# Optimization experiments

Measured on AMD Instinct MI355X. Metric: run time of the kernel, lower is better.

## Reference

```python
import jax, jax.numpy as jnp
import numpy as np

N = 8192
C = 128
K = 20          # neighbors per dilation branch
DILS = (1, 2)   # dilations
K_FULL = K * max(DILS)  # neighbors in the base knn graph
R = 4           # upsampling ratio
N_IDGCN = 2     # inception blocks
NEG_SLOPE_CONV = 0.2
NEG_SLOPE_MLP = 0.01  # torch LeakyReLU default in reconstructor


def knn_idx(pos, k):
    # brute-force knn on [N,3]; exclude self by taking k+1 and dropping col 0
    sq = jnp.sum(pos * pos, axis=-1)                       # [N]
    d = sq[:, None] + sq[None, :] - 2.0 * (pos @ pos.T)    # [N,N]
    _, idx = jax.lax.top_k(-d, k + 1)                      # nearest first
    return idx[:, 1:]                                      # [N,k]


def edge_conv(x, idx, W, b):
    # EdgeConv: max_j LeakyReLU(W @ [x_i, x_j - x_i] + b)
    xj = x[idx]                                            # [N,k,C] gather
    xi = jnp.broadcast_to(x[:, None, :], xj.shape)
    e = jnp.concatenate([xi, xj - xi], axis=-1)            # [N,k,2C]
    h = jax.nn.leaky_relu(e @ W + b, NEG_SLOPE_CONV)
    return jnp.max(h, axis=1)                              # [N,Cout]


def setup_inputs() -> dict:
    key = jax.random.key(0)
    ks = jax.random.split(key, 10)
    s_lift = 1.0 / np.sqrt(6.0)
    s_gcn = 1.0 / np.sqrt(2.0 * C)
    s_mlp = 1.0 / np.sqrt(C)
    n_gcn = N_IDGCN * len(DILS)
    return {
        "x": jax.random.normal(ks[0], (N, 3), dtype=jnp.float32),
        "W0": jax.random.normal(ks[1], (6, C), dtype=jnp.float32) * s_lift,
        "b0": jnp.zeros((C,), dtype=jnp.float32),
        "Wg": jax.random.normal(ks[2], (n_gcn, 2 * C, C), dtype=jnp.float32) * s_gcn,
        "bg": jnp.zeros((n_gcn, C), dtype=jnp.float32),
        "Wu": jax.random.normal(ks[3], (2 * C, R * C), dtype=jnp.float32) * s_gcn,
        "bu": jnp.zeros((R * C,), dtype=jnp.float32),
        "Wr1": jax.random.normal(ks[4], (C, C), dtype=jnp.float32) * s_mlp,
        "br1": jnp.zeros((C,), dtype=jnp.float32),
        "Wr2": jax.random.normal(ks[5], (C, 3), dtype=jnp.float32) * s_mlp,
        "br2": jnp.zeros((3,), dtype=jnp.float32),
    }


def reference(x, W0, b0, Wg, bg, Wu, bu, Wr1, br1, Wr2, br2):
    pos = x
    # knn graph on positions (k * max(dilations) neighbors)
    idx = knn_idx(pos, K_FULL)                             # [N, K_FULL]
    # lift 3 -> C with an EdgeConv on the first K neighbors
    h = edge_conv(pos, idx[:, :K], W0, b0)                 # [N, C]
    # Inception DenseGCN feature extractor: dilated EdgeConv branches + residual
    li = 0
    for _ in range(N_IDGCN):
        acc = jnp.zeros_like(h)
        for d in DILS:
            idx_d = idx[:, ::d][:, :K]                     # dilated neighbors
            acc = acc + edge_conv(h, idx_d, Wg[li], bg[li])
            li += 1
        h = h + acc / float(len(DILS))                     # residual
    # NodeShuffle upsampler: EdgeConv to r*C then shuffle nodes
    u = edge_conv(h, idx[:, :K], Wu, bu)                   # [N, r*C]
    u = u.reshape(N * R, C)                                # [N*r, C]
    # reconstructor MLP -> 3D coordinates
    q = jax.nn.leaky_relu(u @ Wr1 + br1, NEG_SLOPE_MLP)
    q = q @ Wr2 + br2                                      # [N*r, 3]
    return q
```

## Files before the change

### kernel.cpp

```cpp
#include <hip/hip_runtime.h>
#include <math.h>

#define N_PTS 8192
#define KFULL 40
#define KNB 20
#define QB 8
#define NBUCK 1024
#define HWORDS (NBUCK + NBUCK / 16)
#define CAP 384

typedef unsigned short u16;
typedef unsigned int u32;
typedef unsigned long long u64;
typedef __attribute__((ext_vector_type(8))) short bf16x8;
typedef __attribute__((ext_vector_type(4))) float f32x4;

__device__ __forceinline__ u16 f2b(float v) {
  u32 u = __float_as_uint(v);
  return (u16)((u + 0x7FFFu + ((u >> 16) & 1u)) >> 16);
}
__device__ __forceinline__ u32 pk2(float a, float b) {
  return (u32)f2b(a) | ((u32)f2b(b) << 16);
}
__device__ __forceinline__ u32 dmap(float d) {
  u32 b = __float_as_uint(d);
  return b ^ ((u32)(((int)b) >> 31) | 0x80000000u);
}
__device__ __forceinline__ void maxu4(const uint4 v, float m[8]) {
  m[0] = fmaxf(m[0], __uint_as_float(v.x << 16));
  m[1] = fmaxf(m[1], __uint_as_float(v.x & 0xFFFF0000u));
  m[2] = fmaxf(m[2], __uint_as_float(v.y << 16));
  m[3] = fmaxf(m[3], __uint_as_float(v.y & 0xFFFF0000u));
  m[4] = fmaxf(m[4], __uint_as_float(v.z << 16));
  m[5] = fmaxf(m[5], __uint_as_float(v.z & 0xFFFF0000u));
  m[6] = fmaxf(m[6], __uint_as_float(v.w << 16));
  m[7] = fmaxf(m[7], __uint_as_float(v.w & 0xFFFF0000u));
}
__device__ __forceinline__ void unp4(const uint4 v, float p[8]) {
  p[0] = __uint_as_float(v.x << 16);
  p[1] = __uint_as_float(v.x & 0xFFFF0000u);
  p[2] = __uint_as_float(v.y << 16);
  p[3] = __uint_as_float(v.y & 0xFFFF0000u);
  p[4] = __uint_as_float(v.z << 16);
  p[5] = __uint_as_float(v.z & 0xFFFF0000u);
  p[6] = __uint_as_float(v.w << 16);
  p[7] = __uint_as_float(v.w & 0xFFFF0000u);
}

typedef const __attribute__((address_space(1))) unsigned int* gas_p;
typedef __attribute__((address_space(3))) unsigned int* las_p;
__device__ __forceinline__ void gll16(const void* g, void* l) {
  __builtin_amdgcn_global_load_lds((gas_p)g, (las_p)l, 16, 0, 0);
}

__global__ __launch_bounds__(256) void pos4_kernel(const float* __restrict__ pos,
                                                   float4* __restrict__ pos4) {
  const int j = blockIdx.x * 256 + threadIdx.x;
  const float x = pos[j * 3 + 0], y = pos[j * 3 + 1], z = pos[j * 3 + 2];
  pos4[j] = make_float4(x, y, z, x * x + y * y + z * z);
}

__device__ __forceinline__ void scan_cut(const u32 (*hist)[HWORDS], int* s_cut,
                                         int t) {
  const int w = t >> 6, lane = t & 63;
  const u32* H = hist[w];
  const int base = lane * 17;
  u32 lsum = 0;
#pragma unroll
  for (int k = 0; k < 16; ++k) lsum += H[base + k];
  u32 inc = lsum;
#pragma unroll
  for (int off = 1; off < 64; off <<= 1) {
    const u32 u = __shfl_up(inc, off);
    if (lane >= off) inc += u;
  }
  const u32 excl = inc - lsum;
  const u32 TGT = KFULL + 1;
  const u32 exlo = excl & 0xFFFFu, inlo = inc & 0xFFFFu;
  if (exlo < TGT && inlo >= TGT) {
    u32 cum = exlo;
    for (int k = 0; k < 16; ++k) {
      cum += H[base + k] & 0xFFFFu;
      if (cum >= TGT) { s_cut[2 * w] = lane * 16 + k; break; }
    }
  }
  const u32 exhi = excl >> 16, inhi = inc >> 16;
  if (exhi < TGT && inhi >= TGT) {
    u32 cum = exhi;
    for (int k = 0; k < 16; ++k) {
      cum += H[base + k] >> 16;
      if (cum >= TGT) { s_cut[2 * w + 1] = lane * 16 + k; break; }
    }
  }
}

__global__ __launch_bounds__(256) void knn_kernel(const float4* __restrict__ pos4,
                                                  int* __restrict__ idx_out) {
  __shared__ __align__(16) u32 hmem[CAP * QB * 2];
  u32 (*hist)[HWORDS] = (u32(*)[HWORDS])hmem;
  u64 (*cand)[CAP] = (u64(*)[CAP])hmem;
  __shared__ float4 s_q[QB];
  __shared__ int s_cut[QB];
  __shared__ int s_cnt[QB];

  const int qb = blockIdx.x * QB, t = threadIdx.x;
  if (t < QB) {
    s_q[t] = pos4[qb + t];
    s_cnt[t] = 0;
  }
  for (int b = t; b < 4 * HWORDS; b += 256) hmem[b] = 0;
  __syncthreads();

  float qx[QB], qy[QB], qz[QB], qs[QB];
#pragma unroll
  for (int q = 0; q < QB; ++q) {
    const float4 v = s_q[q];
    qx[q] = -2.0f * v.x; qy[q] = -2.0f * v.y; qz[q] = -2.0f * v.z; qs[q] = v.w;
  }

#pragma unroll
  for (int k = 0; k < 2; ++k) {
    const int j = (t + (k << 8)) << 4;
    const float4 p = pos4[j];
#pragma unroll
    for (int q = 0; q < QB; ++q) {
      const float d = fmaf(qx[q], p.x, fmaf(qy[q], p.y, fmaf(qz[q], p.z, qs[q] + p.w)));
      const u32 bk = dmap(d) >> 22;
      atomicAdd(&hist[q >> 1][bk + (bk >> 4)], 1u << ((q & 1) * 16));
    }
  }
  __syncthreads();
  scan_cut(hist, s_cut, t);
  __syncthreads();
  int bcut[QB];
#pragma unroll
  for (int q = 0; q < QB; ++q) bcut[q] = s_cut[q];
  for (int b = t; b < 4 * HWORDS; b += 256) hmem[b] = 0;
  __syncthreads();

  for (int s = 0; s < 32; ++s) {
    const int j = t + (s << 8);
    const float4 p = pos4[j];
#pragma unroll
    for (int q = 0; q < QB; ++q) {
      const float d = fmaf(qx[q], p.x, fmaf(qy[q], p.y, fmaf(qz[q], p.z, qs[q] + p.w)));
      const u32 bk = dmap(d) >> 22;
      if ((int)bk <= bcut[q])
        atomicAdd(&hist[q >> 1][bk + (bk >> 4)], 1u << ((q & 1) * 16));
    }
  }
  __syncthreads();
  scan_cut(hist, s_cut, t);
  __syncthreads();
#pragma unroll
  for (int q = 0; q < QB; ++q) bcut[q] = s_cut[q];
  __syncthreads();

  for (int s = 0; s < 32; ++s) {
    const int j = t + (s << 8);
    const float4 p = pos4[j];
#pragma unroll
    for (int q = 0; q < QB; ++q) {
      const float d = fmaf(qx[q], p.x, fmaf(qy[q], p.y, fmaf(qz[q], p.z, qs[q] + p.w)));
      const u32 mp = dmap(d);
      if ((int)(mp >> 22) <= bcut[q]) {
        const int slot = atomicAdd(&s_cnt[q], 1);
        if (slot < CAP) cand[q][slot] = ((u64)mp << 13) | (u64)j;
      }
    }
  }
  __syncthreads();

  {
    const int w = t >> 6, lane = t & 63;
#pragma unroll
    for (int hh = 0; hh < 2; ++hh) {
      const int q = 2 * w + hh;
      const int cnt = s_cnt[q] < CAP ? s_cnt[q] : CAP;
      for (int c0 = lane; c0 < cnt; c0 += 64) {
        const u64 my = cand[q][c0];
        int rank = 0;
        for (int c = 0; c < cnt; ++c) rank += (cand[q][c] < my) ? 1 : 0;
        if (rank >= 1 && rank <= KFULL)
          idx_out[(qb + q) * KFULL + (rank - 1)] = (int)(my & 0x1FFFull);
      }
    }
  }
}

__global__ __launch_bounds__(128) void lift_kernel(const float* __restrict__ pos,
                                                   const float* __restrict__ W0,
                                                   const float* __restrict__ b0,
                                                   float* __restrict__ Aout,
                                                   u16* __restrict__ Pout) {
  const int i = blockIdx.x;
  const int c = threadIdx.x;
  const float px = pos[i * 3 + 0], py = pos[i * 3 + 1], pz = pos[i * 3 + 2];
  const float a = b0[c] + px * W0[c] + py * W0[128 + c] + pz * W0[256 + c];
  const float p = px * W0[384 + c] + py * W0[512 + c] + pz * W0[640 + c];
  Aout[(size_t)i * 128 + c] = a;
  Pout[(size_t)i * 128 + c] = f2b(p);
}

__global__ __launch_bounds__(128) void wcvt_kernel(const float* __restrict__ src,
                                                   u16* __restrict__ dst, int ncols,
                                                   int rows_per_tensor,
                                                   int elems_per_tensor) {
  const int rg = blockIdx.x;
  const int li = rg / rows_per_tensor;
  const int r = rg % rows_per_tensor;
  const int k = threadIdx.x;
  const float* s = src + (size_t)li * elems_per_tensor;
  u16* d = dst + (size_t)li * elems_per_tensor;
  const int part = r / ncols, col = r % ncols;
  d[(size_t)r * 128 + k] = f2b(s[(size_t)(part * 128 + k) * ncols + col]);
}

__global__ __launch_bounds__(256) void gemm_mfma_kernel(
    const u16* __restrict__ Ain, const u16* __restrict__ Wt,
    const float* __restrict__ bias, int GA, int span_shift, int nAtot, int nPtot,
    float slope, int use_act, float* __restrict__ Aout, u16* __restrict__ Pout) {
  __shared__ __align__(16) u16 Al[128 * 128];
  __shared__ __align__(16) u16 Bl[64 * 128];
  const int bm = blockIdx.x * 128;
  const int bn = blockIdx.y * 64;
  const int tid = threadIdx.x;

#pragma unroll
  for (int it = 0; it < 8; ++it) {
    const int g = it * 256 + tid;
    const int row = g >> 4, cc = g & 15;
    const int sc = cc ^ (row & 7);
    gll16(Ain + (size_t)(bm + row) * 128 + sc * 8, &Al[g * 8]);
  }
#pragma unroll
  for (int it = 0; it < 4; ++it) {
    const int g = it * 256 + tid;
    const int row = g >> 4, cc = g & 15;
    const int sc = cc ^ (row & 7);
    gll16(Wt + (size_t)(bn + row) * 128 + sc * 8, &Bl[g * 8]);
  }
  __syncthreads();

  const int wv = tid >> 6, lane = tid & 63;
  const int wm = wv & 1, wn = wv >> 1;
  const int lr = lane & 15, lk = lane >> 4;

  bf16x8 a[4][4], b[2][4];
  f32x4 acc[4][2];
#pragma unroll
  for (int m = 0; m < 4; ++m)
#pragma unroll
    for (int n = 0; n < 2; ++n) acc[m][n] = (f32x4){0.f, 0.f, 0.f, 0.f};

#pragma unroll
  for (int m = 0; m < 4; ++m) {
    const int row = wm * 64 + m * 16 + lr;
#pragma unroll
    for (int ks = 0; ks < 4; ++ks) {
      const int c = ks * 4 + lk;
      a[m][ks] = *(const bf16x8*)&Al[row * 128 + (c ^ (row & 7)) * 8];
    }
  }
#pragma unroll
  for (int n = 0; n < 2; ++n) {
    const int col = wn * 32 + n * 16 + lr;
#pragma unroll
    for (int ks = 0; ks < 4; ++ks) {
      const int c = ks * 4 + lk;
      b[n][ks] = *(const bf16x8*)&Bl[col * 128 + (c ^ (col & 7)) * 8];
    }
  }

#pragma unroll
  for (int ks = 0; ks < 4; ++ks)
#pragma unroll
    for (int m = 0; m < 4; ++m)
#pragma unroll
      for (int n = 0; n < 2; ++n)
        acc[m][n] = __builtin_amdgcn_mfma_f32_16x16x32_bf16(a[m][ks], b[n][ks],
                                                            acc[m][n], 0, 0, 0);

  const int span = 1 << span_shift;
  const int GP = span - GA;
#pragma unroll
  for (int n = 0; n < 2; ++n) {
    const int col = bn + wn * 32 + n * 16 + lr;
    const int g = col >> span_shift;
    const int wi = col & (span - 1);
    const bool isA = wi < GA;
    const float bv = isA ? bias[g * GA + wi] : 0.f;
#pragma unroll
    for (int m = 0; m < 4; ++m) {
      const int row0 = bm + wm * 64 + m * 16 + lk * 4;
#pragma unroll
      for (int r = 0; r < 4; ++r) {
        float v = acc[m][n][r] + bv;
        if (isA) {
          if (use_act) v = v > 0.f ? v : v * slope;
          Aout[(size_t)(row0 + r) * nAtot + g * GA + wi] = v;
        } else {
          Pout[(size_t)(row0 + r) * nPtot + g * GP + (wi - GA)] = f2b(v);
        }
      }
    }
  }
}

__global__ __launch_bounds__(256) void gather_one_kernel(
    const float* __restrict__ A, const u16* __restrict__ P,
    const int* __restrict__ idx, int C, int dil, float* __restrict__ outf,
    u16* __restrict__ outb) {
  const int t = threadIdx.x;
  const int i = blockIdx.x * 16 + (t >> 4);
  const int c = blockIdx.y * 128 + (t & 15) * 8;
  float m[8];
#pragma unroll
  for (int k = 0; k < 8; ++k) m[k] = -INFINITY;
  const int ib = i * KFULL;
#pragma unroll
  for (int j = 0; j < KNB; ++j) {
    const int n = idx[ib + j * dil] & (N_PTS - 1);
    maxu4(*(const uint4*)&P[(size_t)n * C + c], m);
  }
  float pv[8];
  unp4(*(const uint4*)&P[(size_t)i * C + c], pv);
  const float4 a0 = *(const float4*)&A[(size_t)i * C + c];
  const float4 a1 = *(const float4*)&A[(size_t)i * C + c + 4];
  const float av[8] = {a0.x, a0.y, a0.z, a0.w, a1.x, a1.y, a1.z, a1.w};
  float v[8];
#pragma unroll
  for (int k = 0; k < 8; ++k) {
    const float x = av[k] - pv[k] + m[k];
    v[k] = x > 0.f ? x : 0.2f * x;
  }
  if (outf) {
    *(float4*)&outf[(size_t)i * C + c] = make_float4(v[0], v[1], v[2], v[3]);
    *(float4*)&outf[(size_t)i * C + c + 4] = make_float4(v[4], v[5], v[6], v[7]);
  }
  if (outb) {
    uint4 pb = {pk2(v[0], v[1]), pk2(v[2], v[3]), pk2(v[4], v[5]), pk2(v[6], v[7])};
    *(uint4*)&outb[(size_t)i * C + c] = pb;
  }
}

__global__ __launch_bounds__(256) void gather_pair_kernel(
    const float* __restrict__ Ap, const u16* __restrict__ Pp,
    const int* __restrict__ idx, float* __restrict__ h, u16* __restrict__ hb) {
  const int t = threadIdx.x;
  const int i = blockIdx.x * 16 + (t >> 4);
  const int c = (t & 15) * 8;
  float m1[8], m2[8];
#pragma unroll
  for (int k = 0; k < 8; ++k) { m1[k] = -INFINITY; m2[k] = -INFINITY; }
  const int ib = i * KFULL;
#pragma unroll
  for (int j = 0; j < KNB; ++j) {
    const int n1 = idx[ib + j] & (N_PTS - 1);
    maxu4(*(const uint4*)&Pp[(size_t)n1 * 256 + c], m1);
    const int n2 = idx[ib + 2 * j] & (N_PTS - 1);
    maxu4(*(const uint4*)&Pp[(size_t)n2 * 256 + 128 + c], m2);
  }
  float p0[8], p1[8];
  unp4(*(const uint4*)&Pp[(size_t)i * 256 + c], p0);
  unp4(*(const uint4*)&Pp[(size_t)i * 256 + 128 + c], p1);
  const float4 a00 = *(const float4*)&Ap[(size_t)i * 256 + c];
  const float4 a01 = *(const float4*)&Ap[(size_t)i * 256 + c + 4];
  const float4 a10 = *(const float4*)&Ap[(size_t)i * 256 + 128 + c];
  const float4 a11 = *(const float4*)&Ap[(size_t)i * 256 + 128 + c + 4];
  const float av0[8] = {a00.x, a00.y, a00.z, a00.w, a01.x, a01.y, a01.z, a01.w};
  const float av1[8] = {a10.x, a10.y, a10.z, a10.w, a11.x, a11.y, a11.z, a11.w};
  const float4 h0 = *(const float4*)&h[(size_t)i * 128 + c];
  const float4 h1 = *(const float4*)&h[(size_t)i * 128 + c + 4];
  const float hv[8] = {h0.x, h0.y, h0.z, h0.w, h1.x, h1.y, h1.z, h1.w};
  float v[8];
#pragma unroll
  for (int k = 0; k < 8; ++k) {
    float x1 = av0[k] - p0[k] + m1[k];
    x1 = x1 > 0.f ? x1 : 0.2f * x1;
    float x2 = av1[k] - p1[k] + m2[k];
    x2 = x2 > 0.f ? x2 : 0.2f * x2;
    v[k] = hv[k] + 0.5f * (x1 + x2);
  }
  *(float4*)&h[(size_t)i * 128 + c] = make_float4(v[0], v[1], v[2], v[3]);
  *(float4*)&h[(size_t)i * 128 + c + 4] = make_float4(v[4], v[5], v[6], v[7]);
  uint4 pb = {pk2(v[0], v[1]), pk2(v[2], v[3]), pk2(v[4], v[5]), pk2(v[6], v[7])};
  *(uint4*)&hb[(size_t)i * 128 + c] = pb;
}

__global__ __launch_bounds__(128) void recon2_kernel(const float* __restrict__ T,
                                                     const float* __restrict__ Wr2,
                                                     const float* __restrict__ br2,
                                                     float* __restrict__ out) {
  __shared__ float tile[32][129];
  __shared__ float w2[384];
  const int tid = threadIdx.x;
  const int r0 = blockIdx.x * 32;
  w2[tid] = Wr2[tid];
  w2[tid + 128] = Wr2[tid + 128];
  w2[tid + 256] = Wr2[tid + 256];
  for (int s = 0; s < 32; ++s) tile[s][tid] = T[(size_t)(r0 + s) * 128 + tid];
  __syncthreads();
  if (tid < 96) {
    const int r = tid / 3, n = tid % 3;
    float acc = br2[n];
#pragma unroll
    for (int k = 0; k < 128; ++k) acc = fmaf(tile[r][k], w2[k * 3 + n], acc);
    out[(size_t)(r0 + r) * 3 + n] = acc;
  }
}

extern "C" void kernel_launch(void* const* d_in, const int* in_sizes, int n_in,
                              void* d_out, int out_size, void* d_ws, size_t ws_size,
                              hipStream_t stream) {
  const float* x = (const float*)d_in[0];
  const float* W0 = (const float*)d_in[1];
  const float* b0 = (const float*)d_in[2];
  const float* Wg = (const float*)d_in[3];
  const float* bg = (const float*)d_in[4];
  const float* Wu = (const float*)d_in[5];
  const float* bu = (const float*)d_in[6];
  const float* Wr1 = (const float*)d_in[7];
  const float* br1 = (const float*)d_in[8];
  const float* Wr2 = (const float*)d_in[9];
  const float* br2 = (const float*)d_in[10];
  float* out = (float*)d_out;

  char* w = (char*)d_ws;
  int* idx = (int*)(w + 0);
  float4* pos4 = (float4*)(w + 1310720);
  float* h = (float*)(w + 1441792);
  u16* hb = (u16*)(w + 5636096);
  float* Apair = (float*)(w + 7733248);
  u16* Ppair = (u16*)(w + 16121856);
  u16* Wgb = (u16*)(w + 20316160);
  u16* Wub = (u16*)(w + 20578304);
  u16* Wr1b = (u16*)(w + 20840448);
  float* Abig = (float*)(w + 20873216);
  u16* Pbig = (u16*)(w + 37650432);
  u16* Ub = (u16*)Apair;
  float* T = Abig;

  wcvt_kernel<<<1024, 128, 0, stream>>>(Wg, Wgb, 128, 256, 256 * 128);
  wcvt_kernel<<<1024, 128, 0, stream>>>(Wu, Wub, 512, 1024, 1024 * 128);
  wcvt_kernel<<<128, 128, 0, stream>>>(Wr1, Wr1b, 128, 128, 128 * 128);

  pos4_kernel<<<32, 256, 0, stream>>>(x, pos4);
  knn_kernel<<<N_PTS / QB, 256, 0, stream>>>(pos4, idx);

  lift_kernel<<<N_PTS, 128, 0, stream>>>(x, W0, b0, Abig, Pbig);
  gather_one_kernel<<<dim3(512, 1), 256, 0, stream>>>(Abig, Pbig, idx, 128, 1, h, hb);

  for (int blk = 0; blk < 2; ++blk) {
    const int li = blk * 2;
    gemm_mfma_kernel<<<dim3(64, 8), 256, 0, stream>>>(
        hb, Wgb + (size_t)li * 256 * 128, bg + li * 128, 128, 8, 256, 256, 0.f, 0,
        Apair, Ppair);
    gather_pair_kernel<<<512, 256, 0, stream>>>(Apair, Ppair, idx, h, hb);
  }

  gemm_mfma_kernel<<<dim3(64, 16), 256, 0, stream>>>(hb, Wub, bu, 512, 10, 512, 512,
                                                     0.f, 0, Abig, Pbig);
  gather_one_kernel<<<dim3(512, 4), 256, 0, stream>>>(Abig, Pbig, idx, 512, 1,
                                                      (float*)nullptr, Ub);

  gemm_mfma_kernel<<<dim3(256, 2), 256, 0, stream>>>(Ub, Wr1b, br1, 128, 7, 128, 128,
                                                     0.01f, 1, T, (u16*)nullptr);
  recon2_kernel<<<1024, 128, 0, stream>>>(T, Wr2, br2, out);
}
```

Baseline: 178.1 us.

## Fuse prep kernels and double knn block threads with one query per wave

Measured after the change: 166.3 us. 1.07x faster.

```diff
diff --git a/kernel.cpp b/kernel.cpp
--- a/kernel.cpp
+++ b/kernel.cpp
@@ -5,8 +5,8 @@
 #define KFULL 40
 #define KNB 20
 #define QB 8
+#define KBLK 512
 #define NBUCK 1024
-#define HWORDS (NBUCK + NBUCK / 16)
 #define CAP 384
 
 typedef unsigned short u16;
@@ -53,51 +53,46 @@
   __builtin_amdgcn_global_load_lds((gas_p)g, (las_p)l, 16, 0, 0);
 }
 
-__global__ __launch_bounds__(256) void pos4_kernel(const float* __restrict__ pos,
-                                                   float4* __restrict__ pos4) {
-  const int j = blockIdx.x * 256 + threadIdx.x;
-  const float x = pos[j * 3 + 0], y = pos[j * 3 + 1], z = pos[j * 3 + 2];
-  pos4[j] = make_float4(x, y, z, x * x + y * y + z * z);
-}
-
-__device__ __forceinline__ void scan_cut(const u32 (*hist)[HWORDS], int* s_cut,
+__device__ __forceinline__ void scan_cut(const u32 (*hist)[NBUCK], int* s_cut,
                                          int t) {
   const int w = t >> 6, lane = t & 63;
-  const u32* H = hist[w];
-  const int base = lane * 17;
-  u32 lsum = 0;
-#pragma unroll
-  for (int k = 0; k < 16; ++k) lsum += H[base + k];
-  u32 inc = lsum;
-#pragma unroll
-  for (int off = 1; off < 64; off <<= 1) {
-    const u32 u = __shfl_up(inc, off);
-    if (lane >= off) inc += u;
-  }
-  const u32 excl = inc - lsum;
-  const u32 TGT = KFULL + 1;
-  const u32 exlo = excl & 0xFFFFu, inlo = inc & 0xFFFFu;
-  if (exlo < TGT && inlo >= TGT) {
-    u32 cum = exlo;
-    for (int k = 0; k < 16; ++k) {
-      cum += H[base + k] & 0xFFFFu;
-      if (cum >= TGT) { s_cut[2 * w] = lane * 16 + k; break; }
-    }
-  }
-  const u32 exhi = excl >> 16, inhi = inc >> 16;
-  if (exhi < TGT && inhi >= TGT) {
-    u32 cum = exhi;
-    for (int k = 0; k < 16; ++k) {
-      cum += H[base + k] >> 16;
-      if (cum >= TGT) { s_cut[2 * w + 1] = lane * 16 + k; break; }
-    }
-  }
-}
-
-__global__ __launch_bounds__(256) void knn_kernel(const float4* __restrict__ pos4,
-                                                  int* __restrict__ idx_out) {
+  if (w < QB / 2) {
+    const u32* H = hist[w];
+    const int base = lane * (NBUCK / 64);
+    u32 lsum = 0;
+#pragma unroll
+    for (int k = 0; k < NBUCK / 64; ++k) lsum += H[base + k];
+    u32 inc = lsum;
+#pragma unroll
+    for (int off = 1; off < 64; off <<= 1) {
+      const u32 u = __shfl_up(inc, off);
+      if (lane >= off) inc += u;
+    }
+    const u32 excl = inc - lsum;
+    const u32 TGT = KFULL + 1;
+    const u32 exlo = excl & 0xFFFFu, inlo = inc & 0xFFFFu;
+    if (exlo < TGT && inlo >= TGT) {
+      u32 cum = exlo;
+      for (int k = 0; k < NBUCK / 64; ++k) {
+        cum += H[base + k] & 0xFFFFu;
+        if (cum >= TGT) { s_cut[2 * w] = base + k; break; }
+      }
+    }
+    const u32 exhi = excl >> 16, inhi = inc >> 16;
+    if (exhi < TGT && inhi >= TGT) {
+      u32 cum = exhi;
+      for (int k = 0; k < NBUCK / 64; ++k) {
+        cum += H[base + k] >> 16;
+        if (cum >= TGT) { s_cut[2 * w + 1] = base + k; break; }
+      }
+    }
+  }
+}
+
+__global__ __launch_bounds__(KBLK) void knn_kernel(const float4* __restrict__ pos4,
+                                                   int* __restrict__ idx_out) {
   __shared__ __align__(16) u32 hmem[CAP * QB * 2];
-  u32 (*hist)[HWORDS] = (u32(*)[HWORDS])hmem;
+  u32 (*hist)[NBUCK] = (u32(*)[NBUCK])hmem;
   u64 (*cand)[CAP] = (u64(*)[CAP])hmem;
   __shared__ float4 s_q[QB];
   __shared__ int s_cut[QB];
@@ -108,7 +103,7 @@
     s_q[t] = pos4[qb + t];
     s_cnt[t] = 0;
   }
-  for (int b = t; b < 4 * HWORDS; b += 256) hmem[b] = 0;
+  for (int b = t; b < 4 * NBUCK; b += KBLK) hmem[b] = 0;
   __syncthreads();
 
   float qx[QB], qy[QB], qz[QB], qs[QB];
@@ -118,15 +113,14 @@
     qx[q] = -2.0f * v.x; qy[q] = -2.0f * v.y; qz[q] = -2.0f * v.z; qs[q] = v.w;
   }
 
-#pragma unroll
-  for (int k = 0; k < 2; ++k) {
-    const int j = (t + (k << 8)) << 4;
+  {
+    const int j = t << 4;
     const float4 p = pos4[j];
 #pragma unroll
     for (int q = 0; q < QB; ++q) {
       const float d = fmaf(qx[q], p.x, fmaf(qy[q], p.y, fmaf(qz[q], p.z, qs[q] + p.w)));
       const u32 bk = dmap(d) >> 22;
-      atomicAdd(&hist[q >> 1][bk + (bk >> 4)], 1u << ((q & 1) * 16));
+      atomicAdd(&hist[q >> 1][bk], 1u << ((q & 1) * 16));
     }
   }
   __syncthreads();
@@ -135,18 +129,18 @@
   int bcut[QB];
 #pragma unroll
   for (int q = 0; q < QB; ++q) bcut[q] = s_cut[q];
-  for (int b = t; b < 4 * HWORDS; b += 256) hmem[b] = 0;
-  __syncthreads();
-
-  for (int s = 0; s < 32; ++s) {
-    const int j = t + (s << 8);
+  for (int b = t; b < 4 * NBUCK; b += KBLK) hmem[b] = 0;
+  __syncthreads();
+
+#pragma unroll 2
+  for (int s = 0; s < 16; ++s) {
+    const int j = t + (s << 9);
     const float4 p = pos4[j];
 #pragma unroll
     for (int q = 0; q < QB; ++q) {
       const float d = fmaf(qx[q], p.x, fmaf(qy[q], p.y, fmaf(qz[q], p.z, qs[q] + p.w)));
       const u32 bk = dmap(d) >> 22;
-      if ((int)bk <= bcut[q])
-        atomicAdd(&hist[q >> 1][bk + (bk >> 4)], 1u << ((q & 1) * 16));
+      if ((int)bk <= bcut[q]) atomicAdd(&hist[q >> 1][bk], 1u << ((q & 1) * 16));
     }
   }
   __syncthreads();
@@ -156,8 +150,9 @@
   for (int q = 0; q < QB; ++q) bcut[q] = s_cut[q];
   __syncthreads();
 
-  for (int s = 0; s < 32; ++s) {
-    const int j = t + (s << 8);
+#pragma unroll 2
+  for (int s = 0; s < 16; ++s) {
+    const int j = t + (s << 9);
     const float4 p = pos4[j];
 #pragma unroll
     for (int q = 0; q < QB; ++q) {
@@ -173,47 +168,53 @@
 
   {
     const int w = t >> 6, lane = t & 63;
-#pragma unroll
-    for (int hh = 0; hh < 2; ++hh) {
-      const int q = 2 * w + hh;
-      const int cnt = s_cnt[q] < CAP ? s_cnt[q] : CAP;
-      for (int c0 = lane; c0 < cnt; c0 += 64) {
-        const u64 my = cand[q][c0];
-        int rank = 0;
-        for (int c = 0; c < cnt; ++c) rank += (cand[q][c] < my) ? 1 : 0;
-        if (rank >= 1 && rank <= KFULL)
-          idx_out[(qb + q) * KFULL + (rank - 1)] = (int)(my & 0x1FFFull);
-      }
-    }
-  }
-}
-
-__global__ __launch_bounds__(128) void lift_kernel(const float* __restrict__ pos,
-                                                   const float* __restrict__ W0,
-                                                   const float* __restrict__ b0,
-                                                   float* __restrict__ Aout,
-                                                   u16* __restrict__ Pout) {
-  const int i = blockIdx.x;
-  const int c = threadIdx.x;
-  const float px = pos[i * 3 + 0], py = pos[i * 3 + 1], pz = pos[i * 3 + 2];
-  const float a = b0[c] + px * W0[c] + py * W0[128 + c] + pz * W0[256 + c];
-  const float p = px * W0[384 + c] + py * W0[512 + c] + pz * W0[640 + c];
-  Aout[(size_t)i * 128 + c] = a;
-  Pout[(size_t)i * 128 + c] = f2b(p);
-}
-
-__global__ __launch_bounds__(128) void wcvt_kernel(const float* __restrict__ src,
-                                                   u16* __restrict__ dst, int ncols,
-                                                   int rows_per_tensor,
-                                                   int elems_per_tensor) {
-  const int rg = blockIdx.x;
+    const int cnt = s_cnt[w] < CAP ? s_cnt[w] : CAP;
+    for (int c0 = lane; c0 < cnt; c0 += 64) {
+      const u64 my = cand[w][c0];
+      int rank = 0;
+      for (int c = 0; c < cnt; ++c) rank += (cand[w][c] < my) ? 1 : 0;
+      if (rank >= 1 && rank <= KFULL)
+        idx_out[(qb + w) * KFULL + (rank - 1)] = (int)(my & 0x1FFFull);
+    }
+  }
+}
+
+__device__ __forceinline__ void wcvt_body(const float* __restrict__ src,
+                                          u16* __restrict__ dst, int ncols,
+                                          int rows_per_tensor, int elems_per_tensor,
+                                          int rg, int k) {
   const int li = rg / rows_per_tensor;
   const int r = rg % rows_per_tensor;
-  const int k = threadIdx.x;
   const float* s = src + (size_t)li * elems_per_tensor;
   u16* d = dst + (size_t)li * elems_per_tensor;
   const int part = r / ncols, col = r % ncols;
   d[(size_t)r * 128 + k] = f2b(s[(size_t)(part * 128 + k) * ncols + col]);
+}
+
+__global__ __launch_bounds__(128) void prep_kernel(
+    const float* __restrict__ x, const float* __restrict__ W0,
+    const float* __restrict__ b0, const float* __restrict__ Wg,
+    const float* __restrict__ Wu, const float* __restrict__ Wr1,
+    float* __restrict__ Aout, u16* __restrict__ Pout, u16* __restrict__ Wgb,
+    u16* __restrict__ Wub, u16* __restrict__ Wr1b, float4* __restrict__ pos4) {
+  const int b = blockIdx.x, t = threadIdx.x;
+  if (b < 8192) {
+    const float px = x[b * 3 + 0], py = x[b * 3 + 1], pz = x[b * 3 + 2];
+    const float a = b0[t] + px * W0[t] + py * W0[128 + t] + pz * W0[256 + t];
+    const float p = px * W0[384 + t] + py * W0[512 + t] + pz * W0[640 + t];
+    Aout[(size_t)b * 128 + t] = a;
+    Pout[(size_t)b * 128 + t] = f2b(p);
+  } else if (b < 9216) {
+    wcvt_body(Wg, Wgb, 128, 256, 256 * 128, b - 8192, t);
+  } else if (b < 10240) {
+    wcvt_body(Wu, Wub, 512, 1024, 1024 * 128, b - 9216, t);
+  } else if (b < 10368) {
+    wcvt_body(Wr1, Wr1b, 128, 128, 128 * 128, b - 10240, t);
+  } else {
+    const int j = (b - 10368) * 128 + t;
+    const float px = x[j * 3 + 0], py = x[j * 3 + 1], pz = x[j * 3 + 2];
+    pos4[j] = make_float4(px, py, pz, px * px + py * py + pz * pz);
+  }
 }
 
 __global__ __launch_bounds__(256) void gemm_mfma_kernel(
@@ -441,14 +442,11 @@
   u16* Ub = (u16*)Apair;
   float* T = Abig;
 
-  wcvt_kernel<<<1024, 128, 0, stream>>>(Wg, Wgb, 128, 256, 256 * 128);
-  wcvt_kernel<<<1024, 128, 0, stream>>>(Wu, Wub, 512, 1024, 1024 * 128);
-  wcvt_kernel<<<128, 128, 0, stream>>>(Wr1, Wr1b, 128, 128, 128 * 128);
-
-  pos4_kernel<<<32, 256, 0, stream>>>(x, pos4);
-  knn_kernel<<<N_PTS / QB, 256, 0, stream>>>(pos4, idx);
-
-  lift_kernel<<<N_PTS, 128, 0, stream>>>(x, W0, b0, Abig, Pbig);
+  prep_kernel<<<10432, 128, 0, stream>>>(x, W0, b0, Wg, Wu, Wr1, Abig, Pbig, Wgb,
+                                         Wub, Wr1b, pos4);
+
+  knn_kernel<<<N_PTS / QB, KBLK, 0, stream>>>(pos4, idx);
+
   gather_one_kernel<<<dim3(512, 1), 256, 0, stream>>>(Abig, Pbig, idx, 128, 1, h, hb);
 
   for (int blk = 0; blk < 2; ++blk) {
```
